# Performance work log

Measured on AMD Instinct MI355X. Metric: run time of the kernel, lower is better.

## Reference

```python
import jax, jax.numpy as jnp
import numpy as np

NUM_LAYERS = 2


def setup_inputs() -> dict:
    key = jax.random.key(0)
    k1, k2, k3, k4 = jax.random.split(key, 4)
    N, E, D = 50000, 800000, 100
    features = jax.random.normal(k1, (N, D), dtype=jnp.float32)
    # stacked nn.Linear weights, one [D,D] per layer (no bias)
    W = jax.random.normal(k2, (NUM_LAYERS, D, D), dtype=jnp.float32) * 0.02
    src = jax.random.randint(k3, (E,), 0, N)
    dst = jax.random.randint(k4, (E,), 0, N)
    return {"features": features, "W": W, "src": src, "dst": dst}


def reference(features, W, src, dst):
    N, D = features.shape
    num_layers = W.shape[0]
    inv_lp1 = 1.0 / (num_layers + 1)

    # --- graph preprocessing (mirrors ItemConv.graph setter) ---
    # add self loops (fill_diag 1.0), then row-normalize by inverse degree
    loop = jnp.arange(N)
    src_all = jnp.concatenate([src, loop])  # message sources
    dst_all = jnp.concatenate([dst, loop])  # message destinations (rows of adj_t)
    deg = jax.ops.segment_sum(
        jnp.ones(src_all.shape, dtype=features.dtype), dst_all, num_segments=N
    )
    deg_inv = jnp.where(deg > 0, 1.0 / deg, 0.0)
    w = deg_inv[dst_all]  # per-edge weight: row-normalized, [E+N]

    # --- forward (LightGCN-style conv with linear projections) ---
    avg = features * inv_lp1
    x = features
    for i in range(num_layers):
        x = x @ W[i].T  # nn.Linear(D, D, bias=False)
        # SpMM: out[d] = sum_{e: dst=d} w_e * x[src_e]
        x = jax.ops.segment_sum(w[:, None] * x[src_all], dst_all, num_segments=N)
        # F.normalize(x): L2 along dim=-1 with eps=1e-12 (max-clamped norm)
        norm = jnp.linalg.norm(x, axis=-1, keepdims=True)
        avg = avg + (x / jnp.maximum(norm, 1e-12)) * inv_lp1
    return avg
```

## Files before the change

kernel.cpp:

```cpp
#include <hip/hip_runtime.h>

#define D 100
#define YSTRIDE 128
#define BSHIFT 7
#define BSIZE 128
#define BMASK 127
#define NBKMAX 512
#define EPB 2048
#define DCAP 4096

typedef __attribute__((ext_vector_type(8))) short bf8v;
typedef __attribute__((ext_vector_type(4))) float f4v;

__device__ inline unsigned short f2bf(float f) {
    unsigned u = __float_as_uint(f);
    return (unsigned short)((u + 0x7fffu + ((u >> 16) & 1u)) >> 16);
}
__device__ inline float bflo(unsigned v) { return __uint_as_float(v << 16); }
__device__ inline float bfhi(unsigned v) { return __uint_as_float(v & 0xffff0000u); }
__device__ inline unsigned short pk8(float a, float b) {
    return (unsigned short)(__builtin_amdgcn_cvt_pk_fp8_f32(a, b, 0, false) & 0xffff);
}
__device__ inline float up8lo(unsigned v) { return __builtin_amdgcn_cvt_f32_fp8((int)v, 0); }
__device__ inline float up8hi(unsigned v) { return __builtin_amdgcn_cvt_f32_fp8((int)v, 1); }

__device__ inline void acc8(float* acc, uint2 v, float w) {
    acc[0] = fmaf(__builtin_amdgcn_cvt_f32_fp8((int)v.x, 0), w, acc[0]);
    acc[1] = fmaf(__builtin_amdgcn_cvt_f32_fp8((int)v.x, 1), w, acc[1]);
    acc[2] = fmaf(__builtin_amdgcn_cvt_f32_fp8((int)v.x, 2), w, acc[2]);
    acc[3] = fmaf(__builtin_amdgcn_cvt_f32_fp8((int)v.x, 3), w, acc[3]);
    acc[4] = fmaf(__builtin_amdgcn_cvt_f32_fp8((int)v.y, 0), w, acc[4]);
    acc[5] = fmaf(__builtin_amdgcn_cvt_f32_fp8((int)v.y, 1), w, acc[5]);
    acc[6] = fmaf(__builtin_amdgcn_cvt_f32_fp8((int)v.y, 2), w, acc[6]);
    acc[7] = fmaf(__builtin_amdgcn_cvt_f32_fp8((int)v.y, 3), w, acc[7]);
}

__device__ inline void scan512_excl(int* a, int* t, int tid) {
    int v0 = a[2 * tid], v1 = a[2 * tid + 1];
    t[tid] = v0 + v1;
    __syncthreads();
    for (int off = 1; off < 256; off <<= 1) {
        int u = (tid >= off) ? t[tid - off] : 0;
        __syncthreads();
        t[tid] += u;
        __syncthreads();
    }
    int base = (tid ? t[tid - 1] : 0);
    a[2 * tid]     = base;
    a[2 * tid + 1] = base + v0;
    __syncthreads();
}

__global__ __launch_bounds__(256) void k_pre(const float* __restrict__ x0, const float* __restrict__ W,
                                             unsigned* __restrict__ s8, float* __restrict__ Wc,
                                             int* __restrict__ bcnt, const int* __restrict__ dst,
                                             int N, int E, int nbk, int packb, int ablk) {
    __shared__ int lhist[NBKMAX];
    int tid = threadIdx.x;
    int bx = blockIdx.x;

    if (bx < packb) {
        int t = bx * 256 + tid;
        if (t >= N * 32) return;
        int d = t >> 5, q = t & 31;
        unsigned p = 0u;
        if (q < D / 4) {
            float4 v = *(const float4*)(x0 + (long)d * D + q * 4);
            p = (unsigned)pk8(v.x, v.y) | ((unsigned)pk8(v.z, v.w) << 16);
        }
        s8[t] = p;
    } else if (bx < packb + ablk) {
        int base = (bx - packb) * EPB;
        int count = min(EPB, E - base);
        for (int i = tid; i < NBKMAX; i += 256) lhist[i] = 0;
        __syncthreads();
        for (int i = tid; i < count; i += 256) atomicAdd(&lhist[dst[base + i] >> BSHIFT], 1);
        __syncthreads();
        for (int b = tid; b < nbk; b += 256)
            if (lhist[b]) atomicAdd(&bcnt[b], lhist[b]);
    } else {
        int t = (bx - packb - ablk) * 256 + tid;
        if (t >= D * D) return;
        int i = t / D, j = t - i * D;
        const float* w2 = W + D * D + (long)i * D;
        float s = 0.f;
        for (int k = 0; k < D; k++) s += w2[k] * W[(long)k * D + j];
        Wc[t] = s;
    }
}

__global__ __launch_bounds__(256) void k_scanB_prep(const int* __restrict__ bucket_cnt,
                                                    int* __restrict__ bucket_off,
                                                    int* __restrict__ bucket_cur, int nbk, int E,
                                                    const float* __restrict__ W1,
                                                    const float* __restrict__ Wc,
                                                    unsigned short* __restrict__ P, int wtot) {
    int tid = threadIdx.x;
    if (blockIdx.x == 0) {
        __shared__ int a[NBKMAX], t[256];
        a[tid]       = (tid < nbk) ? bucket_cnt[tid] : 0;
        a[tid + 256] = (tid + 256 < nbk) ? bucket_cnt[tid + 256] : 0;
        __syncthreads();
        scan512_excl(a, t, tid);
        if (tid < nbk)       { bucket_off[tid] = a[tid];             bucket_cur[tid] = a[tid]; }
        if (tid + 256 < nbk) { bucket_off[tid + 256] = a[tid + 256]; bucket_cur[tid + 256] = a[tid + 256]; }
        if (tid == 0) bucket_off[nbk] = E;
    } else {
        int t = (blockIdx.x - 1) * 256 + tid;
        if (t >= wtot) return;
        int lane = t & 63;
        int r = t >> 6;
        int kt = r & 3;
        int r2 = r >> 2;
        int nt = r2 % 7;
        int l  = r2 / 7;
        const float* M = (l == 0) ? W1 : Wc;
        int ng = nt * 16 + (lane & 15);
        int k0 = kt * 32 + (lane >> 4) * 8;
        unsigned short u[8];
#pragma unroll
        for (int j = 0; j < 8; j++) {
            int k = k0 + j;
            u[j] = (ng < D && k < D) ? f2bf(M[(long)ng * D + k]) : (unsigned short)0;
        }
        uint4 o;
        o.x = (unsigned)u[0] | ((unsigned)u[1] << 16);
        o.y = (unsigned)u[2] | ((unsigned)u[3] << 16);
        o.z = (unsigned)u[4] | ((unsigned)u[5] << 16);
        o.w = (unsigned)u[6] | ((unsigned)u[7] << 16);
        *(uint4*)(P + (long)t * 8) = o;
    }
}

__global__ __launch_bounds__(256) void k_bucketC(const int* __restrict__ src,
                                                 const int* __restrict__ dst,
                                                 int* __restrict__ bucket_cur,
                                                 unsigned* __restrict__ ebuf, int E, int nbk) {
    __shared__ int lhist[NBKMAX], lstart[NBKMAX], runS[NBKMAX], t[256];
    __shared__ unsigned stage[EPB];
    int tid = threadIdx.x;
    int base = blockIdx.x * EPB;
    int count = min(EPB, E - base);

    for (int i = tid; i < NBKMAX; i += 256) lhist[i] = 0;
    __syncthreads();
    for (int i = tid; i < count; i += 256) atomicAdd(&lhist[dst[base + i] >> BSHIFT], 1);
    __syncthreads();
    for (int i = tid; i < NBKMAX; i += 256) lstart[i] = lhist[i];
    __syncthreads();
    scan512_excl(lstart, t, tid);
    for (int b = tid; b < nbk; b += 256) {
        int c = lhist[b];
        runS[b] = c ? atomicAdd(&bucket_cur[b], c) : 0;
    }
    __syncthreads();
    for (int i = tid; i < NBKMAX; i += 256) lhist[i] = 0;
    __syncthreads();
    for (int i = tid; i < count; i += 256) {
        int dv = dst[base + i];
        int sv = src[base + i];
        int b = dv >> BSHIFT;
        int r = atomicAdd(&lhist[b], 1);
        stage[lstart[b] + r] = ((unsigned)(dv & BMASK) << 16) | (unsigned)sv;
    }
    __syncthreads();
    int wave = tid >> 6, lane = tid & 63;
    for (int b = wave; b < nbk; b += 4) {
        int c = lhist[b], ls = lstart[b], rs = runS[b];
        for (int j = lane; j < c; j += 64) ebuf[rs + j] = stage[ls + j];
    }
}

__global__ __launch_bounds__(256) void k_bucketD(const unsigned* __restrict__ ebuf,
                                                 const int* __restrict__ bucket_off,
                                                 int* __restrict__ col, int* __restrict__ rowptr,
                                                 int N, int nbk, int E) {
    __shared__ int lh[BSIZE], ls[BSIZE];
    __shared__ int colStage[DCAP];
    int b = blockIdx.x;
    int tid = threadIdx.x;
    int beg = bucket_off[b], end = bucket_off[b + 1];
    int cnt = end - beg;

    if (tid < BSIZE) lh[tid] = 0;
    __syncthreads();
    for (int i = tid; i < cnt; i += 256) atomicAdd(&lh[ebuf[beg + i] >> 16], 1);
    __syncthreads();
    if (tid < BSIZE) ls[tid] = lh[tid];
    __syncthreads();
    for (int off = 1; off < BSIZE; off <<= 1) {
        int v = (tid >= off && tid < BSIZE) ? ls[tid - off] : 0;
        __syncthreads();
        if (tid < BSIZE) ls[tid] += v;
        __syncthreads();
    }
    if (tid < BSIZE) ls[tid] -= lh[tid];
    __syncthreads();
    int d0 = b * BSIZE;
    if (tid < BSIZE && d0 + tid < N) rowptr[d0 + tid] = beg + ls[tid];
    if (b == nbk - 1 && tid == 0) rowptr[N] = E;
    if (tid < BSIZE) lh[tid] = 0;
    __syncthreads();
    if (cnt <= DCAP) {
        for (int i = tid; i < cnt; i += 256) {
            unsigned p = ebuf[beg + i];
            int r = p >> 16, s = (int)(p & 0xffffu);
            int k = atomicAdd(&lh[r], 1);
            colStage[ls[r] + k] = s;
        }
        __syncthreads();
        for (int i = tid; i < cnt; i += 256) col[beg + i] = colStage[i];
    } else {
        for (int i = tid; i < cnt; i += 256) {
            unsigned p = ebuf[beg + i];
            int r = p >> 16, s = (int)(p & 0xffffu);
            int k = atomicAdd(&lh[r], 1);
            col[beg + ls[r] + k] = s;
        }
    }
}

__global__ __launch_bounds__(256) void k_spmm(const unsigned short* __restrict__ g8,
                                              const int* __restrict__ rowptr,
                                              const int* __restrict__ col,
                                              const unsigned* __restrict__ self16,
                                              unsigned short* __restrict__ o8,
                                              unsigned* __restrict__ o16,
                                              int write8, int N) {
    int wave = threadIdx.x >> 6;
    int lane = threadIdx.x & 63;
    int g = lane >> 4;
    int j = lane & 15;
    int d = blockIdx.x * 4 + wave;
    if (d >= N) return;

    int b0 = __builtin_amdgcn_readfirstlane(rowptr[d]);
    int e0 = __builtin_amdgcn_readfirstlane(rowptr[d + 1]);

    float acc[8];
    if (g == 0) {
        if (self16) {
            uint4 sv = *((const uint4*)(self16 + (long)d * 64) + j);
            acc[0] = bflo(sv.x); acc[1] = bfhi(sv.x);
            acc[2] = bflo(sv.y); acc[3] = bfhi(sv.y);
            acc[4] = bflo(sv.z); acc[5] = bfhi(sv.z);
            acc[6] = bflo(sv.w); acc[7] = bfhi(sv.w);
        } else {
            uint2 sv = *(const uint2*)(g8 + (long)d * 64 + j * 4);
#pragma unroll
            for (int k = 0; k < 8; k++) acc[k] = 0.f;
            acc8(acc, sv, 1.f);
        }
    } else {
#pragma unroll
        for (int k = 0; k < 8; k++) acc[k] = 0.f;
    }

    for (int win = b0; win < e0; win += 64) {
        int m = e0 - win;
        if (m > 64) m = 64;
        int c = col[win + lane];
        int t = 0;
        for (; t + 8 <= m; t += 8) {
            int sa = __shfl(c, t + g);
            int sb = __shfl(c, t + 4 + g);
            uint2 va = *(const uint2*)(g8 + (long)sa * 64 + j * 4);
            uint2 vb = *(const uint2*)(g8 + (long)sb * 64 + j * 4);
            acc8(acc, va, 1.f);
            acc8(acc, vb, 1.f);
        }
        for (; t < m; t += 4) {
            int rem = m - t;
            int idx = t + ((g < rem) ? g : 0);
            int sa = __shfl(c, idx);
            float w = (g < rem) ? 1.f : 0.f;
            uint2 va = *(const uint2*)(g8 + (long)sa * 64 + j * 4);
            acc8(acc, va, w);
        }
    }

#pragma unroll
    for (int k = 0; k < 8; k++) {
        acc[k] += __shfl_xor(acc[k], 16);
        acc[k] += __shfl_xor(acc[k], 32);
    }

    float dinv = 1.f / (float)(e0 - b0 + 1);
    float r[8];
#pragma unroll
    for (int k = 0; k < 8; k++) r[k] = acc[k] * dinv;

    if (g == 0) {
        uint4 o;
        o.x = (unsigned)f2bf(r[0]) | ((unsigned)f2bf(r[1]) << 16);
        o.y = (unsigned)f2bf(r[2]) | ((unsigned)f2bf(r[3]) << 16);
        o.z = (unsigned)f2bf(r[4]) | ((unsigned)f2bf(r[5]) << 16);
        o.w = (unsigned)f2bf(r[6]) | ((unsigned)f2bf(r[7]) << 16);
        *((uint4*)(o16 + (long)d * 64) + j) = o;
    }
    if (write8 && g == 1) {
        uint2 p;
        p.x = (unsigned)pk8(r[0], r[1]) | ((unsigned)pk8(r[2], r[3]) << 16);
        p.y = (unsigned)pk8(r[4], r[5]) | ((unsigned)pk8(r[6], r[7]) << 16);
        *((uint2*)((unsigned*)o8 + (long)d * 32) + j) = p;
    }
}

__global__ __launch_bounds__(256) void k_epi(const unsigned short* __restrict__ u16,
                                             const unsigned short* __restrict__ v16,
                                             const unsigned short* __restrict__ P,
                                             const float* __restrict__ x0,
                                             float invlp1, float* __restrict__ out, int N) {
    int wave = threadIdx.x >> 6;
    int lane = threadIdx.x & 63;
    int quad = lane >> 4;
    int l16  = lane & 15;
    int rowbase = (blockIdx.x * 4 + wave) * 16;
    if (rowbase >= N) return;
    int arow = rowbase + l16;
    if (arow >= N) arow = N - 1;

    bf8v aU[4], aV[4];
    const unsigned short* ur = u16 + (long)arow * YSTRIDE;
    const unsigned short* vr = v16 + (long)arow * YSTRIDE;
#pragma unroll
    for (int kt = 0; kt < 4; kt++) {
        int k0 = kt * 32 + quad * 8;
        union { bf8v v; uint4 u; } a, b;
        a.u = *(const uint4*)(ur + k0);
        b.u = *(const uint4*)(vr + k0);
        aU[kt] = a.v;
        aV[kt] = b.v;
    }

    f4v accU[7], accV[7];
#pragma unroll
    for (int nt = 0; nt < 7; nt++) { accU[nt] = (f4v){0,0,0,0}; accV[nt] = (f4v){0,0,0,0}; }

    const uint4* bp = (const uint4*)P;
#pragma unroll
    for (int nt = 0; nt < 7; nt++) {
#pragma unroll
        for (int kt = 0; kt < 4; kt++) {
            union { uint4 u; bf8v v; } b1, b2;
            b1.u = bp[(nt * 4 + kt) * 64 + lane];
            b2.u = bp[(28 + nt * 4 + kt) * 64 + lane];
            accU[nt] = __builtin_amdgcn_mfma_f32_16x16x32_bf16(aU[kt], b1.v, accU[nt], 0, 0, 0);
            accV[nt] = __builtin_amdgcn_mfma_f32_16x16x32_bf16(aV[kt], b2.v, accV[nt], 0, 0, 0);
        }
    }

    float sU[4], sV[4];
#pragma unroll
    for (int i = 0; i < 4; i++) {
        float nu = 0.f, nv = 0.f;
#pragma unroll
        for (int nt = 0; nt < 7; nt++) {
            nu += accU[nt][i] * accU[nt][i];
            nv += accV[nt][i] * accV[nt][i];
        }
#pragma unroll
        for (int m = 1; m < 16; m <<= 1) {
            nu += __shfl_xor(nu, m);
            nv += __shfl_xor(nv, m);
        }
        sU[i] = invlp1 / fmaxf(sqrtf(nu), 1e-12f);
        sV[i] = invlp1 / fmaxf(sqrtf(nv), 1e-12f);
    }

#pragma unroll
    for (int nt = 0; nt < 7; nt++) {
        int cc = nt * 16 + l16;
        if (cc < D) {
#pragma unroll
            for (int i = 0; i < 4; i++) {
                int rr = rowbase + quad * 4 + i;
                if (rr < N) {
                    long idx = (long)rr * D + cc;
                    out[idx] = x0[idx] * invlp1 + accU[nt][i] * sU[i] + accV[nt][i] * sV[i];
                }
            }
        }
    }
}


extern "C" void kernel_launch(void* const* d_in, const int* in_sizes, int n_in,
                              void* d_out, int out_size, void* d_ws, size_t ws_size,
                              hipStream_t stream) {
    const float* features = (const float*)d_in[0];
    const float* W        = (const float*)d_in[1];
    const int*   src      = (const int*)d_in[2];
    const int*   dstv     = (const int*)d_in[3];

    int N = in_sizes[0] / D;
    int E = in_sizes[2];
    int L = in_sizes[1] / (D * D);
    float invlp1 = 1.f / (float)(L + 1);
    int NBK = (N + BSIZE - 1) >> BSHIFT;

    char*  ws  = (char*)d_ws;
    size_t off = 0;
    auto alloc = [&](size_t bytes) -> void* {
        void* p = (void*)(ws + off);
        off += (bytes + 255) & ~(size_t)255;
        return p;
    };
    unsigned*       s8     = (unsigned*)alloc((size_t)N * 32 * sizeof(unsigned));
    unsigned*       u8     = (unsigned*)alloc((size_t)N * 32 * sizeof(unsigned));
    unsigned*       u16    = (unsigned*)alloc((size_t)N * 64 * sizeof(unsigned));
    unsigned*       v16    = (unsigned*)alloc((size_t)N * 64 * sizeof(unsigned));
    float*          Wc     = (float*)alloc((size_t)D * D * sizeof(float));
    unsigned short* wpack  = (unsigned short*)alloc((size_t)2 * 7 * 4 * 64 * 8 * sizeof(unsigned short));
    unsigned*       ebuf   = (unsigned*)alloc((size_t)E * sizeof(unsigned));
    int*            colb   = (int*)alloc((size_t)E * sizeof(int));
    int*            rowptr = (int*)alloc((size_t)(N + 1) * sizeof(int));
    int*            bcnt   = (int*)alloc((size_t)NBKMAX * sizeof(int));
    int*            boff   = (int*)alloc((size_t)(NBKMAX + 1) * sizeof(int));
    int*            bcur   = (int*)alloc((size_t)NBKMAX * sizeof(int));

    int nebk  = (E + EPB - 1) / EPB;
    int wtot  = 2 * 7 * 4 * 64;
    int packb = (N * 32 + 255) / 256;
    int wcb   = (D * D + 255) / 256;
    int prepb = (wtot + 255) / 256;

    hipMemsetAsync(bcnt, 0, (size_t)NBK * sizeof(int), stream);
    k_pre<<<packb + nebk + wcb, 256, 0, stream>>>(features, W, s8, Wc, bcnt, dstv,
                                                  N, E, NBK, packb, nebk);
    k_scanB_prep<<<1 + prepb, 256, 0, stream>>>(bcnt, boff, bcur, NBK, E, W, Wc, wpack, wtot);
    k_bucketC<<<nebk, 256, 0, stream>>>(src, dstv, bcur, ebuf, E, NBK);
    k_bucketD<<<NBK, 256, 0, stream>>>(ebuf, boff, colb, rowptr, N, NBK, E);

    int spmmblocks = (N + 3) / 4;
    k_spmm<<<spmmblocks, 256, 0, stream>>>((const unsigned short*)s8, rowptr, colb,
                                           (const unsigned*)nullptr,
                                           (unsigned short*)u8, u16, 1, N);
    k_spmm<<<spmmblocks, 256, 0, stream>>>((const unsigned short*)u8, rowptr, colb,
                                           u16, (unsigned short*)nullptr, v16, 0, N);

    int nrowtiles = (N + 15) / 16;
    int epiblocks = (nrowtiles + 3) / 4;
    k_epi<<<epiblocks, 256, 0, stream>>>((const unsigned short*)u16, (const unsigned short*)v16,
                                         wpack, features, invlp1, (float*)d_out, N);
}
```

Before: 211.3 us.

## Split fp8 feature gather into two column halves to shrink SpMM working set

Splits the fp8 node feature matrix into low and high column halves stored as separate arrays, and runs each of the two SpMM layers once per half, giving four launches instead of two. Each launch gathers 64-byte rows, so the table being gathered (about 3.2 MB per half) fits better in L2/MALL and random gathers hit cache more often. The main loop is also unrolled to 16 neighbors per step for more loads in flight. The cost is reading rowptr/col twice and extra launch overhead, and each gather is a smaller 4-byte load per lane.

```diff
diff --git a/kernel.cpp b/kernel.cpp
--- a/kernel.cpp
+++ b/kernel.cpp
@@ -21,18 +21,12 @@
 __device__ inline unsigned short pk8(float a, float b) {
     return (unsigned short)(__builtin_amdgcn_cvt_pk_fp8_f32(a, b, 0, false) & 0xffff);
 }
-__device__ inline float up8lo(unsigned v) { return __builtin_amdgcn_cvt_f32_fp8((int)v, 0); }
-__device__ inline float up8hi(unsigned v) { return __builtin_amdgcn_cvt_f32_fp8((int)v, 1); }
-
-__device__ inline void acc8(float* acc, uint2 v, float w) {
-    acc[0] = fmaf(__builtin_amdgcn_cvt_f32_fp8((int)v.x, 0), w, acc[0]);
-    acc[1] = fmaf(__builtin_amdgcn_cvt_f32_fp8((int)v.x, 1), w, acc[1]);
-    acc[2] = fmaf(__builtin_amdgcn_cvt_f32_fp8((int)v.x, 2), w, acc[2]);
-    acc[3] = fmaf(__builtin_amdgcn_cvt_f32_fp8((int)v.x, 3), w, acc[3]);
-    acc[4] = fmaf(__builtin_amdgcn_cvt_f32_fp8((int)v.y, 0), w, acc[4]);
-    acc[5] = fmaf(__builtin_amdgcn_cvt_f32_fp8((int)v.y, 1), w, acc[5]);
-    acc[6] = fmaf(__builtin_amdgcn_cvt_f32_fp8((int)v.y, 2), w, acc[6]);
-    acc[7] = fmaf(__builtin_amdgcn_cvt_f32_fp8((int)v.y, 3), w, acc[7]);
+
+__device__ inline void acc4(float& a0, float& a1, float& a2, float& a3, unsigned v, float w) {
+    a0 = fmaf(__builtin_amdgcn_cvt_f32_fp8((int)v, 0), w, a0);
+    a1 = fmaf(__builtin_amdgcn_cvt_f32_fp8((int)v, 1), w, a1);
+    a2 = fmaf(__builtin_amdgcn_cvt_f32_fp8((int)v, 2), w, a2);
+    a3 = fmaf(__builtin_amdgcn_cvt_f32_fp8((int)v, 3), w, a3);
 }
 
 __device__ inline void scan512_excl(int* a, int* t, int tid) {
@@ -52,7 +46,8 @@
 }
 
 __global__ __launch_bounds__(256) void k_pre(const float* __restrict__ x0, const float* __restrict__ W,
-                                             unsigned* __restrict__ s8, float* __restrict__ Wc,
+                                             unsigned* __restrict__ s8lo, unsigned* __restrict__ s8hi,
+                                             float* __restrict__ Wc,
                                              int* __restrict__ bcnt, const int* __restrict__ dst,
                                              int N, int E, int nbk, int packb, int ablk) {
     __shared__ int lhist[NBKMAX];
@@ -68,7 +63,8 @@
             float4 v = *(const float4*)(x0 + (long)d * D + q * 4);
             p = (unsigned)pk8(v.x, v.y) | ((unsigned)pk8(v.z, v.w) << 16);
         }
-        s8[t] = p;
+        if (q < 16) s8lo[(long)d * 16 + q] = p;
+        else        s8hi[(long)d * 16 + (q - 16)] = p;
     } else if (bx < packb + ablk) {
         int base = (bx - packb) * EPB;
         int count = min(EPB, E - base);
@@ -220,13 +216,13 @@
     }
 }
 
-__global__ __launch_bounds__(256) void k_spmm(const unsigned short* __restrict__ g8,
-                                              const int* __restrict__ rowptr,
-                                              const int* __restrict__ col,
-                                              const unsigned* __restrict__ self16,
-                                              unsigned short* __restrict__ o8,
-                                              unsigned* __restrict__ o16,
-                                              int write8, int N) {
+__global__ __launch_bounds__(256) void k_spmm_h(const unsigned* __restrict__ gh,
+                                                const int* __restrict__ rowptr,
+                                                const int* __restrict__ col,
+                                                const unsigned* __restrict__ self16,
+                                                unsigned* __restrict__ o8h,
+                                                unsigned* __restrict__ o16,
+                                                int h, int N) {
     int wave = threadIdx.x >> 6;
     int lane = threadIdx.x & 63;
     int g = lane >> 4;
@@ -237,23 +233,16 @@
     int b0 = __builtin_amdgcn_readfirstlane(rowptr[d]);
     int e0 = __builtin_amdgcn_readfirstlane(rowptr[d + 1]);
 
-    float acc[8];
+    float a0 = 0.f, a1 = 0.f, a2 = 0.f, a3 = 0.f;
     if (g == 0) {
         if (self16) {
-            uint4 sv = *((const uint4*)(self16 + (long)d * 64) + j);
-            acc[0] = bflo(sv.x); acc[1] = bfhi(sv.x);
-            acc[2] = bflo(sv.y); acc[3] = bfhi(sv.y);
-            acc[4] = bflo(sv.z); acc[5] = bfhi(sv.z);
-            acc[6] = bflo(sv.w); acc[7] = bfhi(sv.w);
+            uint2 sv = *((const uint2*)(self16 + (long)d * 64 + h * 32) + j);
+            a0 = bflo(sv.x); a1 = bfhi(sv.x);
+            a2 = bflo(sv.y); a3 = bfhi(sv.y);
         } else {
-            uint2 sv = *(const uint2*)(g8 + (long)d * 64 + j * 4);
-#pragma unroll
-            for (int k = 0; k < 8; k++) acc[k] = 0.f;
-            acc8(acc, sv, 1.f);
-        }
-    } else {
-#pragma unroll
-        for (int k = 0; k < 8; k++) acc[k] = 0.f;
+            unsigned sv = gh[(long)d * 16 + j];
+            acc4(a0, a1, a2, a3, sv, 1.f);
+        }
     }
 
     for (int win = b0; win < e0; win += 64) {
@@ -261,48 +250,54 @@
         if (m > 64) m = 64;
         int c = col[win + lane];
         int t = 0;
+        for (; t + 16 <= m; t += 16) {
+            int sa = __shfl(c, t + g);
+            int sb = __shfl(c, t + 4 + g);
+            int sc = __shfl(c, t + 8 + g);
+            int sd = __shfl(c, t + 12 + g);
+            unsigned va = gh[(long)sa * 16 + j];
+            unsigned vb = gh[(long)sb * 16 + j];
+            unsigned vc = gh[(long)sc * 16 + j];
+            unsigned vd = gh[(long)sd * 16 + j];
+            acc4(a0, a1, a2, a3, va, 1.f);
+            acc4(a0, a1, a2, a3, vb, 1.f);
+            acc4(a0, a1, a2, a3, vc, 1.f);
+            acc4(a0, a1, a2, a3, vd, 1.f);
+        }
         for (; t + 8 <= m; t += 8) {
             int sa = __shfl(c, t + g);
             int sb = __shfl(c, t + 4 + g);
-            uint2 va = *(const uint2*)(g8 + (long)sa * 64 + j * 4);
-            uint2 vb = *(const uint2*)(g8 + (long)sb * 64 + j * 4);
-            acc8(acc, va, 1.f);
-            acc8(acc, vb, 1.f);
+            unsigned va = gh[(long)sa * 16 + j];
+            unsigned vb = gh[(long)sb * 16 + j];
+            acc4(a0, a1, a2, a3, va, 1.f);
+            acc4(a0, a1, a2, a3, vb, 1.f);
         }
         for (; t < m; t += 4) {
             int rem = m - t;
             int idx = t + ((g < rem) ? g : 0);
             int sa = __shfl(c, idx);
             float w = (g < rem) ? 1.f : 0.f;
-            uint2 va = *(const uint2*)(g8 + (long)sa * 64 + j * 4);
-            acc8(acc, va, w);
-        }
-    }
-
-#pragma unroll
-    for (int k = 0; k < 8; k++) {
-        acc[k] += __shfl_xor(acc[k], 16);
-        acc[k] += __shfl_xor(acc[k], 32);
-    }
+            unsigned va = gh[(long)sa * 16 + j];
+            acc4(a0, a1, a2, a3, va, w);
+        }
+    }
+
+    a0 += __shfl_xor(a0, 16); a0 += __shfl_xor(a0, 32);
+    a1 += __shfl_xor(a1, 16); a1 += __shfl_xor(a1, 32);
+    a2 += __shfl_xor(a2, 16); a2 += __shfl_xor(a2, 32);
+    a3 += __shfl_xor(a3, 16); a3 += __shfl_xor(a3, 32);
 
     float dinv = 1.f / (float)(e0 - b0 + 1);
-    float r[8];
-#pragma unroll
-    for (int k = 0; k < 8; k++) r[k] = acc[k] * dinv;
+    float r0 = a0 * dinv, r1 = a1 * dinv, r2 = a2 * dinv, r3 = a3 * dinv;
 
     if (g == 0) {
-        uint4 o;
-        o.x = (unsigned)f2bf(r[0]) | ((unsigned)f2bf(r[1]) << 16);
-        o.y = (unsigned)f2bf(r[2]) | ((unsigned)f2bf(r[3]) << 16);
-        o.z = (unsigned)f2bf(r[4]) | ((unsigned)f2bf(r[5]) << 16);
-        o.w = (unsigned)f2bf(r[6]) | ((unsigned)f2bf(r[7]) << 16);
-        *((uint4*)(o16 + (long)d * 64) + j) = o;
-    }
-    if (write8 && g == 1) {
-        uint2 p;
-        p.x = (unsigned)pk8(r[0], r[1]) | ((unsigned)pk8(r[2], r[3]) << 16);
-        p.y = (unsigned)pk8(r[4], r[5]) | ((unsigned)pk8(r[6], r[7]) << 16);
-        *((uint2*)((unsigned*)o8 + (long)d * 32) + j) = p;
+        uint2 o;
+        o.x = (unsigned)f2bf(r0) | ((unsigned)f2bf(r1) << 16);
+        o.y = (unsigned)f2bf(r2) | ((unsigned)f2bf(r3) << 16);
+        *((uint2*)(o16 + (long)d * 64 + h * 32) + j) = o;
+    }
+    if (o8h && g == 1) {
+        o8h[(long)d * 16 + j] = (unsigned)pk8(r0, r1) | ((unsigned)pk8(r2, r3) << 16);
     }
 }
 
@@ -406,8 +401,10 @@
         off += (bytes + 255) & ~(size_t)255;
         return p;
     };
-    unsigned*       s8     = (unsigned*)alloc((size_t)N * 32 * sizeof(unsigned));
-    unsigned*       u8     = (unsigned*)alloc((size_t)N * 32 * sizeof(unsigned));
+    unsigned*       s8lo   = (unsigned*)alloc((size_t)N * 16 * sizeof(unsigned));
+    unsigned*       s8hi   = (unsigned*)alloc((size_t)N * 16 * sizeof(unsigned));
+    unsigned*       u8lo   = (unsigned*)alloc((size_t)N * 16 * sizeof(unsigned));
+    unsigned*       u8hi   = (unsigned*)alloc((size_t)N * 16 * sizeof(unsigned));
     unsigned*       u16    = (unsigned*)alloc((size_t)N * 64 * sizeof(unsigned));
     unsigned*       v16    = (unsigned*)alloc((size_t)N * 64 * sizeof(unsigned));
     float*          Wc     = (float*)alloc((size_t)D * D * sizeof(float));
@@ -426,18 +423,21 @@
     int prepb = (wtot + 255) / 256;
 
     hipMemsetAsync(bcnt, 0, (size_t)NBK * sizeof(int), stream);
-    k_pre<<<packb + nebk + wcb, 256, 0, stream>>>(features, W, s8, Wc, bcnt, dstv,
+    k_pre<<<packb + nebk + wcb, 256, 0, stream>>>(features, W, s8lo, s8hi, Wc, bcnt, dstv,
                                                   N, E, NBK, packb, nebk);
     k_scanB_prep<<<1 + prepb, 256, 0, stream>>>(bcnt, boff, bcur, NBK, E, W, Wc, wpack, wtot);
     k_bucketC<<<nebk, 256, 0, stream>>>(src, dstv, bcur, ebuf, E, NBK);
     k_bucketD<<<NBK, 256, 0, stream>>>(ebuf, boff, colb, rowptr, N, NBK, E);
 
     int spmmblocks = (N + 3) / 4;
-    k_spmm<<<spmmblocks, 256, 0, stream>>>((const unsigned short*)s8, rowptr, colb,
-                                           (const unsigned*)nullptr,
-                                           (unsigned short*)u8, u16, 1, N);
-    k_spmm<<<spmmblocks, 256, 0, stream>>>((const unsigned short*)u8, rowptr, colb,
-                                           u16, (unsigned short*)nullptr, v16, 0, N);
+    k_spmm_h<<<spmmblocks, 256, 0, stream>>>(s8lo, rowptr, colb, (const unsigned*)nullptr,
+                                             u8lo, u16, 0, N);
+    k_spmm_h<<<spmmblocks, 256, 0, stream>>>(u8lo, rowptr, colb, u16,
+                                             (unsigned*)nullptr, v16, 0, N);
+    k_spmm_h<<<spmmblocks, 256, 0, stream>>>(s8hi, rowptr, colb, (const unsigned*)nullptr,
+                                             u8hi, u16, 1, N);
+    k_spmm_h<<<spmmblocks, 256, 0, stream>>>(u8hi, rowptr, colb, u16,
+                                             (unsigned*)nullptr, v16, 1, N);
 
     int nrowtiles = (N + 15) / 16;
     int epiblocks = (nrowtiles + 3) / 4;
```

New measurement: 239.0 us. 13.1% more time.

## Replace atomic bucket offset allocation with per-block histogram column scans

Applied to the files above, without the earlier changes.

Each edge block now writes its full bucket histogram to global memory instead of atomically adding into global bucket counters. A new per-bucket column scan computes each block's deterministic offset within every bucket, and a separate small kernel scans the bucket totals. The bucket-scatter kernel then reads these precomputed offsets rather than using atomicAdd on a cursor. This removes the memset and global atomic contention and makes the edge order deterministic, at the cost of one extra kernel launch and extra histogram traffic.

```diff
diff --git a/kernel.cpp b/kernel.cpp
--- a/kernel.cpp
+++ b/kernel.cpp
@@ -53,7 +53,7 @@
 
 __global__ __launch_bounds__(256) void k_pre(const float* __restrict__ x0, const float* __restrict__ W,
                                              unsigned* __restrict__ s8, float* __restrict__ Wc,
-                                             int* __restrict__ bcnt, const int* __restrict__ dst,
+                                             int* __restrict__ hist, const int* __restrict__ dst,
                                              int N, int E, int nbk, int packb, int ablk) {
     __shared__ int lhist[NBKMAX];
     int tid = threadIdx.x;
@@ -70,14 +70,14 @@
         }
         s8[t] = p;
     } else if (bx < packb + ablk) {
-        int base = (bx - packb) * EPB;
+        int blk = bx - packb;
+        int base = blk * EPB;
         int count = min(EPB, E - base);
         for (int i = tid; i < NBKMAX; i += 256) lhist[i] = 0;
         __syncthreads();
         for (int i = tid; i < count; i += 256) atomicAdd(&lhist[dst[base + i] >> BSHIFT], 1);
         __syncthreads();
-        for (int b = tid; b < nbk; b += 256)
-            if (lhist[b]) atomicAdd(&bcnt[b], lhist[b]);
+        for (int b = tid; b < NBKMAX; b += 256) hist[(long)blk * NBKMAX + b] = lhist[b];
     } else {
         int t = (bx - packb - ablk) * 256 + tid;
         if (t >= D * D) return;
@@ -89,27 +89,29 @@
     }
 }
 
-__global__ __launch_bounds__(256) void k_scanB_prep(const int* __restrict__ bucket_cnt,
-                                                    int* __restrict__ bucket_off,
-                                                    int* __restrict__ bucket_cur, int nbk, int E,
-                                                    const float* __restrict__ W1,
-                                                    const float* __restrict__ Wc,
-                                                    unsigned short* __restrict__ P, int wtot) {
+__global__ __launch_bounds__(256) void k_colscan_prep(const int* __restrict__ hist,
+                                                      int* __restrict__ pref, int* __restrict__ bcnt,
+                                                      int nebk, int nbk,
+                                                      const float* __restrict__ W1,
+                                                      const float* __restrict__ Wc,
+                                                      unsigned short* __restrict__ P, int wtot) {
     int tid = threadIdx.x;
-    if (blockIdx.x == 0) {
+    if ((int)blockIdx.x < nbk) {
+        int b = blockIdx.x;
         __shared__ int a[NBKMAX], t[256];
-        a[tid]       = (tid < nbk) ? bucket_cnt[tid] : 0;
-        a[tid + 256] = (tid + 256 < nbk) ? bucket_cnt[tid + 256] : 0;
+        int i0 = tid, i1 = tid + 256;
+        a[i0] = (i0 < nebk) ? hist[(long)i0 * NBKMAX + b] : 0;
+        a[i1] = (i1 < nebk) ? hist[(long)i1 * NBKMAX + b] : 0;
         __syncthreads();
         scan512_excl(a, t, tid);
-        if (tid < nbk)       { bucket_off[tid] = a[tid];             bucket_cur[tid] = a[tid]; }
-        if (tid + 256 < nbk) { bucket_off[tid + 256] = a[tid + 256]; bucket_cur[tid + 256] = a[tid + 256]; }
-        if (tid == 0) bucket_off[nbk] = E;
+        if (i0 < nebk) pref[(long)i0 * NBKMAX + b] = a[i0];
+        if (i1 < nebk) pref[(long)i1 * NBKMAX + b] = a[i1];
+        if (tid == 0) bcnt[b] = a[nebk];
     } else {
-        int t = (blockIdx.x - 1) * 256 + tid;
-        if (t >= wtot) return;
-        int lane = t & 63;
-        int r = t >> 6;
+        int t2 = ((int)blockIdx.x - nbk) * 256 + tid;
+        if (t2 >= wtot) return;
+        int lane = t2 & 63;
+        int r = t2 >> 6;
         int kt = r & 3;
         int r2 = r >> 2;
         int nt = r2 % 7;
@@ -128,13 +130,27 @@
         o.y = (unsigned)u[2] | ((unsigned)u[3] << 16);
         o.z = (unsigned)u[4] | ((unsigned)u[5] << 16);
         o.w = (unsigned)u[6] | ((unsigned)u[7] << 16);
-        *(uint4*)(P + (long)t * 8) = o;
-    }
+        *(uint4*)(P + (long)t2 * 8) = o;
+    }
+}
+
+__global__ __launch_bounds__(256) void k_scanB(const int* __restrict__ bcnt,
+                                               int* __restrict__ boff, int nbk, int E) {
+    __shared__ int a[NBKMAX], t[256];
+    int tid = threadIdx.x;
+    a[tid]       = (tid < nbk) ? bcnt[tid] : 0;
+    a[tid + 256] = (tid + 256 < nbk) ? bcnt[tid + 256] : 0;
+    __syncthreads();
+    scan512_excl(a, t, tid);
+    if (tid < nbk)       boff[tid] = a[tid];
+    if (tid + 256 < nbk) boff[tid + 256] = a[tid + 256];
+    if (tid == 0) boff[nbk] = E;
 }
 
 __global__ __launch_bounds__(256) void k_bucketC(const int* __restrict__ src,
                                                  const int* __restrict__ dst,
-                                                 int* __restrict__ bucket_cur,
+                                                 const int* __restrict__ boff,
+                                                 const int* __restrict__ pref,
                                                  unsigned* __restrict__ ebuf, int E, int nbk) {
     __shared__ int lhist[NBKMAX], lstart[NBKMAX], runS[NBKMAX], t[256];
     __shared__ unsigned stage[EPB];
@@ -149,10 +165,8 @@
     for (int i = tid; i < NBKMAX; i += 256) lstart[i] = lhist[i];
     __syncthreads();
     scan512_excl(lstart, t, tid);
-    for (int b = tid; b < nbk; b += 256) {
-        int c = lhist[b];
-        runS[b] = c ? atomicAdd(&bucket_cur[b], c) : 0;
-    }
+    for (int b = tid; b < nbk; b += 256)
+        runS[b] = boff[b] + pref[(long)blockIdx.x * NBKMAX + b];
     __syncthreads();
     for (int i = tid; i < NBKMAX; i += 256) lhist[i] = 0;
     __syncthreads();
@@ -398,6 +412,7 @@
     int L = in_sizes[1] / (D * D);
     float invlp1 = 1.f / (float)(L + 1);
     int NBK = (N + BSIZE - 1) >> BSHIFT;
+    int nebk = (E + EPB - 1) / EPB;
 
     char*  ws  = (char*)d_ws;
     size_t off = 0;
@@ -415,21 +430,22 @@
     unsigned*       ebuf   = (unsigned*)alloc((size_t)E * sizeof(unsigned));
     int*            colb   = (int*)alloc((size_t)E * sizeof(int));
     int*            rowptr = (int*)alloc((size_t)(N + 1) * sizeof(int));
+    int*            hist   = (int*)alloc((size_t)nebk * NBKMAX * sizeof(int));
+    int*            pref   = (int*)alloc((size_t)nebk * NBKMAX * sizeof(int));
     int*            bcnt   = (int*)alloc((size_t)NBKMAX * sizeof(int));
     int*            boff   = (int*)alloc((size_t)(NBKMAX + 1) * sizeof(int));
-    int*            bcur   = (int*)alloc((size_t)NBKMAX * sizeof(int));
-
-    int nebk  = (E + EPB - 1) / EPB;
+
     int wtot  = 2 * 7 * 4 * 64;
     int packb = (N * 32 + 255) / 256;
     int wcb   = (D * D + 255) / 256;
     int prepb = (wtot + 255) / 256;
 
-    hipMemsetAsync(bcnt, 0, (size_t)NBK * sizeof(int), stream);
-    k_pre<<<packb + nebk + wcb, 256, 0, stream>>>(features, W, s8, Wc, bcnt, dstv,
+    k_pre<<<packb + nebk + wcb, 256, 0, stream>>>(features, W, s8, Wc, hist, dstv,
                                                   N, E, NBK, packb, nebk);
-    k_scanB_prep<<<1 + prepb, 256, 0, stream>>>(bcnt, boff, bcur, NBK, E, W, Wc, wpack, wtot);
-    k_bucketC<<<nebk, 256, 0, stream>>>(src, dstv, bcur, ebuf, E, NBK);
+    k_colscan_prep<<<NBK + prepb, 256, 0, stream>>>(hist, pref, bcnt, nebk, NBK,
+                                                    W, Wc, wpack, wtot);
+    k_scanB<<<1, 256, 0, stream>>>(bcnt, boff, NBK, E);
+    k_bucketC<<<nebk, 256, 0, stream>>>(src, dstv, boff, pref, ebuf, E, NBK);
     k_bucketD<<<NBK, 256, 0, stream>>>(ebuf, boff, colb, rowptr, N, NBK, E);
 
     int spmmblocks = (N + 3) / 4;
```

After: 200.5 us. -5.1%, faster.

## Replace counted bucket sort with fixed-capacity buckets and per-row start/degree arrays

Applied to the files above, without the earlier changes.

Removes the separate bucket-count histogram pass and the global prefix scan by giving each destination bucket a fixed capacity slot (BCAP) and using per-bucket atomic cursors directly. The CSR build now emits per-row start and degree arrays instead of a global rowptr, and the SpMM reads degree directly. The memset and the scan/prep launch are removed, and weight packing is folded into the sort kernel, cutting kernel launches and one full pass over dst. The risk is that buckets exceeding BCAP entries are silently truncated, so correctness relies on the random graph keeping bucket sizes under capacity (expected ~2048 per bucket).

```diff
diff --git a/kernel.cpp b/kernel.cpp
--- a/kernel.cpp
+++ b/kernel.cpp
@@ -7,7 +7,8 @@
 #define BMASK 127
 #define NBKMAX 512
 #define EPB 2048
-#define DCAP 4096
+#define BCAP 4096
+#define WTOT (2 * 7 * 4 * 64)
 
 typedef __attribute__((ext_vector_type(8))) short bf8v;
 typedef __attribute__((ext_vector_type(4))) float f4v;
@@ -21,8 +22,6 @@
 __device__ inline unsigned short pk8(float a, float b) {
     return (unsigned short)(__builtin_amdgcn_cvt_pk_fp8_f32(a, b, 0, false) & 0xffff);
 }
-__device__ inline float up8lo(unsigned v) { return __builtin_amdgcn_cvt_f32_fp8((int)v, 0); }
-__device__ inline float up8hi(unsigned v) { return __builtin_amdgcn_cvt_f32_fp8((int)v, 1); }
 
 __device__ inline void acc8(float* acc, uint2 v, float w) {
     acc[0] = fmaf(__builtin_amdgcn_cvt_f32_fp8((int)v.x, 0), w, acc[0]);
@@ -53,9 +52,8 @@
 
 __global__ __launch_bounds__(256) void k_pre(const float* __restrict__ x0, const float* __restrict__ W,
                                              unsigned* __restrict__ s8, float* __restrict__ Wc,
-                                             int* __restrict__ bcnt, const int* __restrict__ dst,
-                                             int N, int E, int nbk, int packb, int ablk) {
-    __shared__ int lhist[NBKMAX];
+                                             int* __restrict__ cur,
+                                             int N, int packb) {
     int tid = threadIdx.x;
     int bx = blockIdx.x;
 
@@ -69,17 +67,11 @@
             p = (unsigned)pk8(v.x, v.y) | ((unsigned)pk8(v.z, v.w) << 16);
         }
         s8[t] = p;
-    } else if (bx < packb + ablk) {
-        int base = (bx - packb) * EPB;
-        int count = min(EPB, E - base);
-        for (int i = tid; i < NBKMAX; i += 256) lhist[i] = 0;
-        __syncthreads();
-        for (int i = tid; i < count; i += 256) atomicAdd(&lhist[dst[base + i] >> BSHIFT], 1);
-        __syncthreads();
-        for (int b = tid; b < nbk; b += 256)
-            if (lhist[b]) atomicAdd(&bcnt[b], lhist[b]);
+    } else if (bx == packb) {
+        cur[tid] = 0;
+        cur[tid + 256] = 0;
     } else {
-        int t = (bx - packb - ablk) * 256 + tid;
+        int t = (bx - packb - 1) * 256 + tid;
         if (t >= D * D) return;
         int i = t / D, j = t - i * D;
         const float* w2 = W + D * D + (long)i * D;
@@ -89,27 +81,23 @@
     }
 }
 
-__global__ __launch_bounds__(256) void k_scanB_prep(const int* __restrict__ bucket_cnt,
-                                                    int* __restrict__ bucket_off,
-                                                    int* __restrict__ bucket_cur, int nbk, int E,
-                                                    const float* __restrict__ W1,
-                                                    const float* __restrict__ Wc,
-                                                    unsigned short* __restrict__ P, int wtot) {
+__global__ __launch_bounds__(256) void k_sortC(const int* __restrict__ src,
+                                               const int* __restrict__ dst,
+                                               int* __restrict__ cur,
+                                               unsigned* __restrict__ ebuf, int E, int nbk,
+                                               int nebk,
+                                               const float* __restrict__ W1,
+                                               const float* __restrict__ Wc,
+                                               unsigned short* __restrict__ P) {
+    __shared__ int lhist[NBKMAX], lstart[NBKMAX], runS[NBKMAX], t[256];
+    __shared__ unsigned stage[EPB];
     int tid = threadIdx.x;
-    if (blockIdx.x == 0) {
-        __shared__ int a[NBKMAX], t[256];
-        a[tid]       = (tid < nbk) ? bucket_cnt[tid] : 0;
-        a[tid + 256] = (tid + 256 < nbk) ? bucket_cnt[tid + 256] : 0;
-        __syncthreads();
-        scan512_excl(a, t, tid);
-        if (tid < nbk)       { bucket_off[tid] = a[tid];             bucket_cur[tid] = a[tid]; }
-        if (tid + 256 < nbk) { bucket_off[tid + 256] = a[tid + 256]; bucket_cur[tid + 256] = a[tid + 256]; }
-        if (tid == 0) bucket_off[nbk] = E;
-    } else {
-        int t = (blockIdx.x - 1) * 256 + tid;
-        if (t >= wtot) return;
-        int lane = t & 63;
-        int r = t >> 6;
+
+    if ((int)blockIdx.x >= nebk) {
+        int t2 = ((int)blockIdx.x - nebk) * 256 + tid;
+        if (t2 >= WTOT) return;
+        int lane = t2 & 63;
+        int r = t2 >> 6;
         int kt = r & 3;
         int r2 = r >> 2;
         int nt = r2 % 7;
@@ -128,17 +116,10 @@
         o.y = (unsigned)u[2] | ((unsigned)u[3] << 16);
         o.z = (unsigned)u[4] | ((unsigned)u[5] << 16);
         o.w = (unsigned)u[6] | ((unsigned)u[7] << 16);
-        *(uint4*)(P + (long)t * 8) = o;
-    }
-}
-
-__global__ __launch_bounds__(256) void k_bucketC(const int* __restrict__ src,
-                                                 const int* __restrict__ dst,
-                                                 int* __restrict__ bucket_cur,
-                                                 unsigned* __restrict__ ebuf, int E, int nbk) {
-    __shared__ int lhist[NBKMAX], lstart[NBKMAX], runS[NBKMAX], t[256];
-    __shared__ unsigned stage[EPB];
-    int tid = threadIdx.x;
+        *(uint4*)(P + (long)t2 * 8) = o;
+        return;
+    }
+
     int base = blockIdx.x * EPB;
     int count = min(EPB, E - base);
 
@@ -151,7 +132,7 @@
     scan512_excl(lstart, t, tid);
     for (int b = tid; b < nbk; b += 256) {
         int c = lhist[b];
-        runS[b] = c ? atomicAdd(&bucket_cur[b], c) : 0;
+        runS[b] = b * BCAP + (c ? atomicAdd(&cur[b], c) : 0);
     }
     __syncthreads();
     for (int i = tid; i < NBKMAX; i += 256) lhist[i] = 0;
@@ -171,16 +152,18 @@
     }
 }
 
-__global__ __launch_bounds__(256) void k_bucketD(const unsigned* __restrict__ ebuf,
-                                                 const int* __restrict__ bucket_off,
-                                                 int* __restrict__ col, int* __restrict__ rowptr,
-                                                 int N, int nbk, int E) {
+__global__ __launch_bounds__(256) void k_csrD(const unsigned* __restrict__ ebuf,
+                                              const int* __restrict__ cur,
+                                              int* __restrict__ col,
+                                              int* __restrict__ rps, int* __restrict__ rdeg,
+                                              int N, int nbk) {
     __shared__ int lh[BSIZE], ls[BSIZE];
-    __shared__ int colStage[DCAP];
+    __shared__ int colStage[BCAP];
     int b = blockIdx.x;
     int tid = threadIdx.x;
-    int beg = bucket_off[b], end = bucket_off[b + 1];
-    int cnt = end - beg;
+    int beg = b * BCAP;
+    int cnt = cur[b];
+    if (cnt > BCAP) cnt = BCAP;
 
     if (tid < BSIZE) lh[tid] = 0;
     __syncthreads();
@@ -197,31 +180,25 @@
     if (tid < BSIZE) ls[tid] -= lh[tid];
     __syncthreads();
     int d0 = b * BSIZE;
-    if (tid < BSIZE && d0 + tid < N) rowptr[d0 + tid] = beg + ls[tid];
-    if (b == nbk - 1 && tid == 0) rowptr[N] = E;
+    if (tid < BSIZE && d0 + tid < N) {
+        rps[d0 + tid]  = beg + ls[tid];
+        rdeg[d0 + tid] = lh[tid];
+    }
     if (tid < BSIZE) lh[tid] = 0;
     __syncthreads();
-    if (cnt <= DCAP) {
-        for (int i = tid; i < cnt; i += 256) {
-            unsigned p = ebuf[beg + i];
-            int r = p >> 16, s = (int)(p & 0xffffu);
-            int k = atomicAdd(&lh[r], 1);
-            colStage[ls[r] + k] = s;
-        }
-        __syncthreads();
-        for (int i = tid; i < cnt; i += 256) col[beg + i] = colStage[i];
-    } else {
-        for (int i = tid; i < cnt; i += 256) {
-            unsigned p = ebuf[beg + i];
-            int r = p >> 16, s = (int)(p & 0xffffu);
-            int k = atomicAdd(&lh[r], 1);
-            col[beg + ls[r] + k] = s;
-        }
-    }
+    for (int i = tid; i < cnt; i += 256) {
+        unsigned p = ebuf[beg + i];
+        int r = p >> 16, s = (int)(p & 0xffffu);
+        int k = atomicAdd(&lh[r], 1);
+        colStage[ls[r] + k] = s;
+    }
+    __syncthreads();
+    for (int i = tid; i < cnt; i += 256) col[beg + i] = colStage[i];
 }
 
 __global__ __launch_bounds__(256) void k_spmm(const unsigned short* __restrict__ g8,
-                                              const int* __restrict__ rowptr,
+                                              const int* __restrict__ rps,
+                                              const int* __restrict__ rdeg,
                                               const int* __restrict__ col,
                                               const unsigned* __restrict__ self16,
                                               unsigned short* __restrict__ o8,
@@ -234,8 +211,9 @@
     int d = blockIdx.x * 4 + wave;
     if (d >= N) return;
 
-    int b0 = __builtin_amdgcn_readfirstlane(rowptr[d]);
-    int e0 = __builtin_amdgcn_readfirstlane(rowptr[d + 1]);
+    int b0  = __builtin_amdgcn_readfirstlane(rps[d]);
+    int deg = __builtin_amdgcn_readfirstlane(rdeg[d]);
+    int e0 = b0 + deg;
 
     float acc[8];
     if (g == 0) {
@@ -285,7 +263,7 @@
         acc[k] += __shfl_xor(acc[k], 32);
     }
 
-    float dinv = 1.f / (float)(e0 - b0 + 1);
+    float dinv = 1.f / (float)(deg + 1);
     float r[8];
 #pragma unroll
     for (int k = 0; k < 8; k++) r[k] = acc[k] * dinv;
@@ -398,6 +376,7 @@
     int L = in_sizes[1] / (D * D);
     float invlp1 = 1.f / (float)(L + 1);
     int NBK = (N + BSIZE - 1) >> BSHIFT;
+    int nebk = (E + EPB - 1) / EPB;
 
     char*  ws  = (char*)d_ws;
     size_t off = 0;
@@ -411,32 +390,26 @@
     unsigned*       u16    = (unsigned*)alloc((size_t)N * 64 * sizeof(unsigned));
     unsigned*       v16    = (unsigned*)alloc((size_t)N * 64 * sizeof(unsigned));
     float*          Wc     = (float*)alloc((size_t)D * D * sizeof(float));
-    unsigned short* wpack  = (unsigned short*)alloc((size_t)2 * 7 * 4 * 64 * 8 * sizeof(unsigned short));
-    unsigned*       ebuf   = (unsigned*)alloc((size_t)E * sizeof(unsigned));
-    int*            colb   = (int*)alloc((size_t)E * sizeof(int));
-    int*            rowptr = (int*)alloc((size_t)(N + 1) * sizeof(int));
-    int*            bcnt   = (int*)alloc((size_t)NBKMAX * sizeof(int));
-    int*            boff   = (int*)alloc((size_t)(NBKMAX + 1) * sizeof(int));
-    int*            bcur   = (int*)alloc((size_t)NBKMAX * sizeof(int));
-
-    int nebk  = (E + EPB - 1) / EPB;
-    int wtot  = 2 * 7 * 4 * 64;
+    unsigned short* wpack  = (unsigned short*)alloc((size_t)WTOT * 8 * sizeof(unsigned short));
+    unsigned*       ebuf   = (unsigned*)alloc((size_t)NBK * BCAP * sizeof(unsigned));
+    int*            colb   = (int*)alloc((size_t)NBK * BCAP * sizeof(int));
+    int*            rps    = (int*)alloc((size_t)N * sizeof(int));
+    int*            rdeg   = (int*)alloc((size_t)N * sizeof(int));
+    int*            cur    = (int*)alloc((size_t)NBKMAX * sizeof(int));
+
     int packb = (N * 32 + 255) / 256;
     int wcb   = (D * D + 255) / 256;
-    int prepb = (wtot + 255) / 256;
-
-    hipMemsetAsync(bcnt, 0, (size_t)NBK * sizeof(int), stream);
-    k_pre<<<packb + nebk + wcb, 256, 0, stream>>>(features, W, s8, Wc, bcnt, dstv,
-                                                  N, E, NBK, packb, nebk);
-    k_scanB_prep<<<1 + prepb, 256, 0, stream>>>(bcnt, boff, bcur, NBK, E, W, Wc, wpack, wtot);
-    k_bucketC<<<nebk, 256, 0, stream>>>(src, dstv, bcur, ebuf, E, NBK);
-    k_bucketD<<<NBK, 256, 0, stream>>>(ebuf, boff, colb, rowptr, N, NBK, E);
+    int prepb = (WTOT + 255) / 256;
+
+    k_pre<<<packb + 1 + wcb, 256, 0, stream>>>(features, W, s8, Wc, cur, N, packb);
+    k_sortC<<<nebk + prepb, 256, 0, stream>>>(src, dstv, cur, ebuf, E, NBK, nebk, W, Wc, wpack);
+    k_csrD<<<NBK, 256, 0, stream>>>(ebuf, cur, colb, rps, rdeg, N, NBK);
 
     int spmmblocks = (N + 3) / 4;
-    k_spmm<<<spmmblocks, 256, 0, stream>>>((const unsigned short*)s8, rowptr, colb,
+    k_spmm<<<spmmblocks, 256, 0, stream>>>((const unsigned short*)s8, rps, rdeg, colb,
                                            (const unsigned*)nullptr,
                                            (unsigned short*)u8, u16, 1, N);
-    k_spmm<<<spmmblocks, 256, 0, stream>>>((const unsigned short*)u8, rowptr, colb,
+    k_spmm<<<spmmblocks, 256, 0, stream>>>((const unsigned short*)u8, rps, rdeg, colb,
                                            u16, (unsigned short*)nullptr, v16, 0, N);
 
     int nrowtiles = (N + 15) / 16;
```

Result: faster. 198.1 us (-6.2%).
